# Performance work log

Hardware: AMD Instinct MI355X
Metric: run time of the kernel (lower is better)

The kernel has to match this reference:

```python
import jax, jax.numpy as jnp
import numpy as np
import math

HID = 768
HEADS = 12
HEAD_DIM = HID // HEADS
B, L = 64, 1024


def _xavier(key, shape):
    fan_in, fan_out = shape[0], shape[1]
    lim = math.sqrt(6.0 / (fan_in + fan_out))
    return jax.random.uniform(key, shape, jnp.float32, -lim, lim)


def setup_inputs() -> dict:
    key = jax.random.key(0)
    ks = jax.random.split(key, 12)
    inp = {
        "x_img": jax.random.normal(ks[0], (B, L, HID), jnp.float32),
        "cond": jax.random.normal(ks[1], (B, HID), jnp.float32),
        # attention projections
        "wq": _xavier(ks[2], (HID, HID)), "bq": jnp.zeros((HID,), jnp.float32),
        "wk": _xavier(ks[3], (HID, HID)), "bk": jnp.zeros((HID,), jnp.float32),
        "wv": _xavier(ks[4], (HID, HID)), "bv": jnp.zeros((HID,), jnp.float32),
        "wo": _xavier(ks[5], (HID, HID)), "bo": jnp.zeros((HID,), jnp.float32),
        # adaLN: zero-initialized in the original (keep small random so grads are non-trivial? No — stay faithful: zero init is the module's init, but zero would kill modulation. Use small random for a meaningful test.)
        "w_ada": jax.random.normal(ks[6], (HID, 6 * HID), jnp.float32) * 0.02,
        "b_ada": jnp.zeros((6 * HID,), jnp.float32),
        # MLP
        "w1": _xavier(ks[7], (HID, HID)), "b1": jnp.zeros((HID,), jnp.float32),
        "w2": _xavier(ks[8], (HID, HID)), "b2": jnp.zeros((HID,), jnp.float32),
        # LayerNorm params (norm_1: default scale=1, bias init const 1; norm_2: scale init const 1, bias default 0)
        "ln1_scale": jnp.ones((HID,), jnp.float32), "ln1_bias": jnp.ones((HID,), jnp.float32),
        "ln2_scale": jnp.ones((HID,), jnp.float32), "ln2_bias": jnp.zeros((HID,), jnp.float32),
    }
    return inp


def _layernorm(x, scale, bias, eps=1e-6):
    mu = jnp.mean(x, axis=-1, keepdims=True)
    var = jnp.var(x, axis=-1, keepdims=True)
    return (x - mu) * jax.lax.rsqrt(var + eps) * scale + bias


def _modulate(x, shift, scale):
    # shift/scale: [B, H] -> broadcast over seq axis
    return x * (1.0 + scale[:, None, :]) + shift[:, None, :]


def _attention(x, wq, bq, wk, bk, wv, bv, wo, bo):
    q = x @ wq + bq
    k = x @ wk + bk
    v = x @ wv + bv
    def split(t):
        b, l, _ = t.shape
        return t.reshape(b, l, HEADS, HEAD_DIM).transpose(0, 2, 1, 3)  # b h l d
    q, k, v = split(q), split(k), split(v)
    logits = jnp.einsum("bhqd,bhkd->bhqk", q, k) / math.sqrt(HEAD_DIM)
    attn = jax.nn.softmax(logits, axis=-1)
    out = jnp.einsum("bhqk,bhkd->bhqd", attn, v)
    out = out.transpose(0, 2, 1, 3).reshape(x.shape)  # b l (h d)
    return out @ wo + bo


def reference(x_img, cond, wq, bq, wk, bk, wv, bv, wo, bo, w_ada, b_ada,
              w1, b1, w2, b2, ln1_scale, ln1_bias, ln2_scale, ln2_bias):
    c = jax.nn.silu(cond) @ w_ada + b_ada  # [B, 6H]
    shift_msa, scale_msa, gate_msa, shift_mlp, scale_mlp, gate_mlp = jnp.split(c, 6, axis=1)

    h = _modulate(_layernorm(x_img, ln1_scale, ln1_bias), shift_msa, scale_msa)
    attn_out = _attention(h, wq, bq, wk, bk, wv, bv, wo, bo)
    x = x_img + gate_msa[:, None, :] * attn_out

    h2 = _modulate(_layernorm(x, ln2_scale, ln2_bias), shift_mlp, scale_mlp)
    mlp_out = jax.nn.silu(h2 @ w1 + b1) @ w2 + b2
    x = x + gate_mlp[:, None, :] * mlp_out
    return x
```

## Files before the change

### kernel.cpp

```cpp
#include <hip/hip_runtime.h>
#include <hip/hip_bf16.h>

typedef __bf16 bf16x8 __attribute__((ext_vector_type(8)));
typedef __bf16 bf16x4 __attribute__((ext_vector_type(4)));
typedef float  f32x4  __attribute__((ext_vector_type(4)));

#define MFMA_BF16(A_, B_, C_) __builtin_amdgcn_mfma_f32_16x16x32_bf16(A_, B_, C_, 0, 0, 0)

static constexpr int    HIDC  = 768;
static constexpr int    BB    = 64;
static constexpr int    LL    = 1024;
static constexpr int    MROWS = BB * LL;
static constexpr int    NHEAD = 12;
static constexpr int    HD    = 64;
static constexpr size_t QKV1  = (size_t)BB * NHEAD * LL * HD;
static constexpr float  QSCALE = 0.1803368801111204f;

static constexpr size_t OFF_WQKVT = 0;
static constexpr size_t OFF_WOT   = OFF_WQKVT + (size_t)2304 * 768 * 2;
static constexpr size_t OFF_W1T   = OFF_WOT   + (size_t)768 * 768 * 2;
static constexpr size_t OFF_W2T   = OFF_W1T   + (size_t)768 * 768 * 2;
static constexpr size_t OFF_BQKV  = OFF_W2T   + (size_t)768 * 768 * 2;
static constexpr size_t OFF_C     = OFF_BQKV  + (size_t)2304 * 4;
static constexpr size_t OFF_H     = OFF_C     + (size_t)64 * 4608 * 4;
static constexpr size_t OFF_AO    = OFF_H     + (size_t)MROWS * HIDC * 2;
static constexpr size_t OFF_QKV   = OFF_AO    + (size_t)MROWS * HIDC * 2;

__device__ __forceinline__ void async16(const __bf16* g, __bf16* l) {
    __builtin_amdgcn_global_load_lds((const __attribute__((address_space(1))) void*)g,
                                     (__attribute__((address_space(3))) void*)l, 16, 0, 0);
}

#define PH_BARRIER() do { __builtin_amdgcn_sched_barrier(0); asm volatile("" ::: "memory"); \
    __builtin_amdgcn_s_barrier(); asm volatile("" ::: "memory"); __builtin_amdgcn_sched_barrier(0); } while (0)
#define SYNC() do { asm volatile("" ::: "memory"); __builtin_amdgcn_s_barrier(); \
                    asm volatile("" ::: "memory"); } while (0)

__global__ __launch_bounds__(256) void tcvt6_k(const float* __restrict__ s0, const float* __restrict__ s1,
                                               const float* __restrict__ s2, const float* __restrict__ s3,
                                               const float* __restrict__ s4, const float* __restrict__ s5,
                                               __bf16* __restrict__ dbase) {
    __shared__ float t[64][65];
    const int bid = blockIdx.x;
    const int widx = bid / 144;
    const int tb = bid - widx * 144;
    const int kt = tb / 12, nt = tb - kt * 12;
    const float* src = (widx == 0) ? s0 : (widx == 1) ? s1 : (widx == 2) ? s2
                     : (widx == 3) ? s3 : (widx == 4) ? s4 : s5;
    const int tid = threadIdx.x;
    const int r = tid >> 4, c4 = (tid & 15) * 4;
    #pragma unroll
    for (int i = 0; i < 4; ++i) {
        const float4 v = *(const float4*)(src + (size_t)(kt * 64 + r + 16 * i) * 768 + nt * 64 + c4);
        t[r + 16 * i][c4 + 0] = v.x; t[r + 16 * i][c4 + 1] = v.y;
        t[r + 16 * i][c4 + 2] = v.z; t[r + 16 * i][c4 + 3] = v.w;
    }
    __syncthreads();
    const int n = tid >> 2, kg = (tid & 3) * 8;
    #pragma unroll
    for (int i = 0; i < 2; ++i) {
        const int k = kg + i * 32;
        bf16x8 o;
        #pragma unroll
        for (int j = 0; j < 8; ++j) o[j] = (__bf16)t[k + j][n];
        *(bf16x8*)(dbase + (size_t)widx * 768 * 768 + (size_t)(nt * 64 + n) * 768 + kt * 64 + k) = o;
    }
}

__global__ __launch_bounds__(256) void bcat_k(const float* __restrict__ bq, const float* __restrict__ bk,
                                              const float* __restrict__ bv, float* __restrict__ bqkv) {
    int i = blockIdx.x * 256 + threadIdx.x;
    if (i < 2304) {
        int w = i / 768, r = i - w * 768;
        const float* p = (w == 0) ? bq : (w == 1) ? bk : bv;
        bqkv[i] = p[r];
    }
}

__global__ __launch_bounds__(256) void ada_k(const float* __restrict__ cond, const float* __restrict__ w_ada,
                                             const float* __restrict__ b_ada, float* __restrict__ c) {
    __shared__ float s[8][768];
    const int tid = threadIdx.x;
    const int bt = blockIdx.x / 18;
    const int nt = blockIdx.x % 18;
    #pragma unroll
    for (int i = 0; i < 24; ++i) {
        int idx = i * 256 + tid;
        int bb = idx / 768, kk = idx - bb * 768;
        float v = cond[(size_t)(bt * 8 + bb) * 768 + kk];
        s[bb][kk] = v / (1.f + __expf(-v));
    }
    __syncthreads();
    const int n = nt * 256 + tid;
    float acc[8];
    #pragma unroll
    for (int j = 0; j < 8; ++j) acc[j] = 0.f;
    for (int k = 0; k < 768; ++k) {
        float w = w_ada[(size_t)k * 4608 + n];
        #pragma unroll
        for (int j = 0; j < 8; ++j) acc[j] += s[j][k] * w;
    }
    float bias = b_ada[n];
    #pragma unroll
    for (int j = 0; j < 8; ++j) c[(size_t)(bt * 8 + j) * 4608 + n] = acc[j] + bias;
}

__global__ __launch_bounds__(256) void ln_mod_f4_k(const float* __restrict__ x,
                                                   const float* __restrict__ lns, const float* __restrict__ lnb,
                                                   const float* __restrict__ c, int shift_off, int scale_off,
                                                   __bf16* __restrict__ out) {
    const int wave = threadIdx.x >> 6, lane = threadIdx.x & 63;
    const int row = blockIdx.x * 4 + wave;
    const size_t base = (size_t)row * HIDC;
    const int b = row >> 10;
    float4 v[3];
    #pragma unroll
    for (int i = 0; i < 3; ++i) v[i] = *(const float4*)(x + base + (i * 64 + lane) * 4);
    float s = 0.f, ss = 0.f;
    #pragma unroll
    for (int i = 0; i < 3; ++i) {
        s  += v[i].x + v[i].y + v[i].z + v[i].w;
        ss += v[i].x * v[i].x + v[i].y * v[i].y + v[i].z * v[i].z + v[i].w * v[i].w;
    }
    #pragma unroll
    for (int off = 1; off < 64; off <<= 1) { s += __shfl_xor(s, off); ss += __shfl_xor(ss, off); }
    const float mu   = s * (1.f / 768.f);
    const float var  = ss * (1.f / 768.f) - mu * mu;
    const float rstd = rsqrtf(var + 1e-6f);
    const float* cb = c + (size_t)b * 4608;
    #pragma unroll
    for (int i = 0; i < 3; ++i) {
        bf16x4 o;
        const float vv[4] = {v[i].x, v[i].y, v[i].z, v[i].w};
        #pragma unroll
        for (int j = 0; j < 4; ++j) {
            const int col = (i * 64 + lane) * 4 + j;
            float val = (vv[j] - mu) * rstd * lns[col] + lnb[col];
            val = val * (1.f + cb[scale_off + col]) + cb[shift_off + col];
            o[j] = (__bf16)val;
        }
        *(bf16x4*)(out + base + (i * 64 + lane) * 4) = o;
    }
}

__global__ __launch_bounds__(256) void ln_mod_b_k(const __bf16* __restrict__ x,
                                                  const float* __restrict__ lns, const float* __restrict__ lnb,
                                                  const float* __restrict__ c, int shift_off, int scale_off,
                                                  __bf16* __restrict__ out) {
    const int wave = threadIdx.x >> 6, lane = threadIdx.x & 63;
    const int row = blockIdx.x * 4 + wave;
    const size_t base = (size_t)row * HIDC;
    const int b = row >> 10;
    float v[12];
    #pragma unroll
    for (int i = 0; i < 3; ++i) {
        const bf16x4 xv = *(const bf16x4*)(x + base + (i * 64 + lane) * 4);
        #pragma unroll
        for (int j = 0; j < 4; ++j) v[i * 4 + j] = (float)xv[j];
    }
    float s = 0.f, ss = 0.f;
    #pragma unroll
    for (int i = 0; i < 12; ++i) { s += v[i]; ss += v[i] * v[i]; }
    #pragma unroll
    for (int off = 1; off < 64; off <<= 1) { s += __shfl_xor(s, off); ss += __shfl_xor(ss, off); }
    const float mu   = s * (1.f / 768.f);
    const float var  = ss * (1.f / 768.f) - mu * mu;
    const float rstd = rsqrtf(var + 1e-6f);
    const float* cb = c + (size_t)b * 4608;
    #pragma unroll
    for (int i = 0; i < 3; ++i) {
        bf16x4 o;
        #pragma unroll
        for (int j = 0; j < 4; ++j) {
            const int col = (i * 64 + lane) * 4 + j;
            float val = (v[i * 4 + j] - mu) * rstd * lns[col] + lnb[col];
            val = val * (1.f + cb[scale_off + col]) + cb[shift_off + col];
            o[j] = (__bf16)val;
        }
        *(bf16x4*)(out + base + (i * 64 + lane) * 4) = o;
    }
}

template<int EPI>
__global__ __launch_bounds__(512, 2) void gemm256_k(const __bf16* __restrict__ A, const __bf16* __restrict__ BT,
                                                    const float* __restrict__ bias, int NBLK,
                                                    const float* __restrict__ e_res, const __bf16* __restrict__ e_resb,
                                                    const float* __restrict__ e_gate, void* __restrict__ out0) {
    constexpr int K = 768;
    constexpr int NKT = K / 64;
    __shared__ __attribute__((aligned(16))) unsigned char LDSB[131072];
    const int tid = threadIdx.x;
    const int nwg = gridDim.x;
    const int cpx = nwg >> 3;
    const int bid = blockIdx.x;
    const int swz = (bid & 7) * cpx + (bid >> 3);
    const int mb = swz / NBLK, nb = swz - mb * NBLK;
    const size_t m0 = (size_t)mb * 256;
    const int n0 = nb * 256;
    const int wave = tid >> 6, lane = tid & 63;
    const int wm = wave >> 2, wn = wave & 3;
    const int lr = lane & 15, lg = lane >> 4;

    int prow[2], pcol[2], pphys[2];
    #pragma unroll
    for (int i = 0; i < 2; ++i) {
        int p = (i * 512 + tid) * 16;
        prow[i]  = p >> 7;
        pcol[i]  = ((p & 127) ^ ((prow[i] & 7) << 4)) >> 1;
        pphys[i] = p;
    }
    auto STAGE = [&](const __bf16* gbase, size_t rowstart, int kt, int regoff) {
        #pragma unroll
        for (int i = 0; i < 2; ++i) {
            const __bf16* g = gbase + (rowstart + (size_t)prow[i]) * K + kt * 64 + pcol[i];
            async16(g, (__bf16*)(LDSB + regoff + pphys[i]));
        }
    };
    auto AFRAG = [&](int db, int mf, int ks) -> bf16x8 {
        const int row = mf * 16 + lr;
        const int ph = row * 128 + ((ks * 64 + lg * 16) ^ ((row & 7) << 4));
        return *(const bf16x8*)(LDSB + db * 65536 + wm * 16384 + ph);
    };
    auto BFRAG = [&](int db, int nf, int ks) -> bf16x8 {
        const int row = (wn & 1) * 64 + nf * 16 + lr;
        const int ph = row * 128 + ((ks * 64 + lg * 16) ^ ((row & 7) << 4));
        return *(const bf16x8*)(LDSB + db * 65536 + 32768 + (wn >> 1) * 16384 + ph);
    };

    f32x4 acc[8][4];
    #pragma unroll
    for (int i = 0; i < 8; ++i)
        #pragma unroll
        for (int j = 0; j < 4; ++j) acc[i][j] = (f32x4){0.f, 0.f, 0.f, 0.f};
    bf16x8 Af[4][2], Af2[4][2], Bf[4][2];

    STAGE(BT, (size_t)n0,       0, 32768);
    STAGE(BT, (size_t)n0 + 128, 0, 49152);
    STAGE(A,  m0,               0, 0);
    STAGE(A,  m0 + 128,         0, 16384);
    STAGE(BT, (size_t)n0,       1, 65536 + 32768);
    STAGE(BT, (size_t)n0 + 128, 1, 65536 + 49152);
    asm volatile("s_waitcnt vmcnt(4)" ::: "memory");
    PH_BARRIER();

    #pragma unroll 2
    for (int g = 0; g < NKT; ++g) {
        const int db = g & 1, dbn = db ^ 1;
        #pragma unroll
        for (int mf = 0; mf < 4; ++mf) { Af[mf][0] = AFRAG(db, mf, 0); Af[mf][1] = AFRAG(db, mf, 1); }
        #pragma unroll
        for (int nf = 0; nf < 4; ++nf) { Bf[nf][0] = BFRAG(db, nf, 0); Bf[nf][1] = BFRAG(db, nf, 1); }
        if (g + 1 < NKT) {
            STAGE(A, m0,       g + 1, dbn * 65536);
            STAGE(A, m0 + 128, g + 1, dbn * 65536 + 16384);
        }
        __builtin_amdgcn_s_setprio(1);
        #pragma unroll
        for (int ks = 0; ks < 2; ++ks)
            #pragma unroll
            for (int mf = 0; mf < 4; ++mf)
                #pragma unroll
                for (int nf = 0; nf < 4; ++nf)
                    acc[mf][nf] = MFMA_BF16(Af[mf][ks], Bf[nf][ks], acc[mf][nf]);
        __builtin_amdgcn_s_setprio(0);
        PH_BARRIER();
        #pragma unroll
        for (int mf = 0; mf < 4; ++mf) { Af2[mf][0] = AFRAG(db, mf + 4, 0); Af2[mf][1] = AFRAG(db, mf + 4, 1); }
        if (g + 2 < NKT) {
            STAGE(BT, (size_t)n0,       g + 2, db * 65536 + 32768);
            STAGE(BT, (size_t)n0 + 128, g + 2, db * 65536 + 49152);
        }
        __builtin_amdgcn_s_setprio(1);
        #pragma unroll
        for (int ks = 0; ks < 2; ++ks)
            #pragma unroll
            for (int mf = 0; mf < 4; ++mf)
                #pragma unroll
                for (int nf = 0; nf < 4; ++nf)
                    acc[mf + 4][nf] = MFMA_BF16(Af2[mf][ks], Bf[nf][ks], acc[mf + 4][nf]);
        __builtin_amdgcn_s_setprio(0);
        if (g < NKT - 2)       asm volatile("s_waitcnt vmcnt(4)" ::: "memory");
        else if (g == NKT - 2) asm volatile("s_waitcnt vmcnt(0)" ::: "memory");
        if (g + 1 < NKT) PH_BARRIER();
    }

    #pragma unroll
    for (int mf = 0; mf < 8; ++mf) {
        #pragma unroll
        for (int nf = 0; nf < 4; ++nf) {
            const int col = wn * 64 + nf * 16 + lr;
            const int n = n0 + col;
            const int row0 = wm * 128 + mf * 16 + lg * 4;
            const size_t mbase = m0 + row0;
            float v4[4];
            #pragma unroll
            for (int r = 0; r < 4; ++r) v4[r] = acc[mf][nf][r] + bias[n];
            if constexpr (EPI == 0) {
                const int which = n / 768, rem = n - which * 768;
                const int hh = rem >> 6, dd = rem & 63;
                const size_t bI = mbase >> 10;
                const size_t lI0 = mbase & 1023;
                if (which == 0) {
                    #pragma unroll
                    for (int r = 0; r < 4; ++r)
                        ((__bf16*)out0)[(((size_t)bI * NHEAD + hh) * LL + lI0 + r) * HD + dd] = (__bf16)(v4[r] * QSCALE);
                } else if (which == 1) {
                    #pragma unroll
                    for (int r = 0; r < 4; ++r)
                        ((__bf16*)out0)[QKV1 + (((size_t)bI * NHEAD + hh) * LL + lI0 + r) * HD + dd] = (__bf16)v4[r];
                } else {
                    const int tile = (int)(lI0 >> 6), kv = (int)(lI0 & 63);
                    const int ks = kv >> 5, r5 = kv & 31;
                    const int lgj = (r5 >> 2) & 3;
                    const int jb = (r5 >> 4) << 2;
                    const int of = dd >> 4, lr2 = dd & 15;
                    bf16x4 pk;
                    #pragma unroll
                    for (int r = 0; r < 4; ++r) pk[r] = (__bf16)v4[r];
                    *(bf16x4*)((__bf16*)out0 + 2 * QKV1 + ((size_t)bI * NHEAD + hh) * (LL * HD)
                               + (size_t)tile * 4096 + ((ks * 4 + of) * 64 + lgj * 16 + lr2) * 8 + jb) = pk;
                }
            } else {
                #pragma unroll
                for (int r = 0; r < 4; ++r) {
                    const size_t m = mbase + r;
                    if constexpr (EPI == 2) {
                        float sv = v4[r] / (1.f + __expf(-v4[r]));
                        ((__bf16*)out0)[m * HIDC + n] = (__bf16)sv;
                    } else if constexpr (EPI == 3) {
                        size_t bI = m >> 10;
                        float gg = e_gate[bI * 4608 + n];
                        ((__bf16*)out0)[m * HIDC + n] = (__bf16)(e_res[m * HIDC + n] + gg * v4[r]);
                    } else {
                        size_t bI = m >> 10;
                        float gg = e_gate[bI * 4608 + n];
                        ((float*)out0)[m * HIDC + n] = (float)e_resb[m * HIDC + n] + gg * v4[r];
                    }
                }
            }
        }
    }
}

__global__ __launch_bounds__(512, 4) void attn_k(const __bf16* __restrict__ qb, const __bf16* __restrict__ kb,
                                                 const __bf16* __restrict__ v2g, __bf16* __restrict__ out) {
    __shared__ __attribute__((aligned(16))) unsigned char LDSA[32768];
    const int nwg = gridDim.x;
    const int cpx = nwg >> 3;
    const int bid = blockIdx.x;
    const int swz = (bid & 7) * cpx + (bid >> 3);
    const int bh = swz >> 2;
    const int qt = swz & 3;
    const int b = bh / NHEAD, h = bh - b * NHEAD;
    const int tid = threadIdx.x;
    const int wave = tid >> 6, lane = tid & 63;
    const int lr = lane & 15, lg = lane >> 4;
    const size_t base = (size_t)bh * LL * HD;

    const int q0 = qt * 256 + wave * 32;
    bf16x8 qf[2][2];
    #pragma unroll
    for (int qi = 0; qi < 2; ++qi) {
        const __bf16* qrow = qb + base + (size_t)(q0 + qi * 16 + lr) * HD;
        qf[qi][0] = *(const bf16x8*)(qrow + lg * 8);
        qf[qi][1] = *(const bf16x8*)(qrow + 32 + lg * 8);
    }

    const int pp = tid * 16;
    const int krow = pp >> 7;
    const int kcol = (pp & 127) ^ ((krow & 7) << 4);
    auto STAGE = [&](int t) {
        unsigned char* Lb = LDSA + (t & 1) * 16384;
        const __bf16* gk = kb + base + (size_t)(t * 64 + krow) * HD + (kcol >> 1);
        async16(gk, (__bf16*)(Lb + pp));
        const __bf16* gv = v2g + base + (size_t)t * 4096 + (pp >> 1);
        async16(gv, (__bf16*)(Lb + 8192 + pp));
    };

    bf16x8 vones;
    #pragma unroll
    for (int j = 0; j < 8; ++j) vones[j] = (__bf16)1.0f;

    f32x4 acc[2][4];
    f32x4 accl[2];
    #pragma unroll
    for (int qi = 0; qi < 2; ++qi) {
        accl[qi] = (f32x4){0.f, 0.f, 0.f, 0.f};
        #pragma unroll
        for (int i = 0; i < 4; ++i) acc[qi][i] = (f32x4){0.f, 0.f, 0.f, 0.f};
    }

    STAGE(0);

    for (int t = 0; t < LL / 64; ++t) {
        asm volatile("s_waitcnt vmcnt(0)" ::: "memory");
        SYNC();
        if (t + 1 < LL / 64) STAGE(t + 1);
        const unsigned char* KB = LDSA + (t & 1) * 16384;
        const unsigned char* VB = KB + 8192;

        f32x4 s[2][4];
        __builtin_amdgcn_s_setprio(1);
        #pragma unroll
        for (int sf = 0; sf < 4; ++sf) {
            const int row = sf * 16 + lr;
            const bf16x8 kf0 = *(const bf16x8*)(KB + row * 128 + ((lg * 16) ^ ((row & 7) << 4)));
            const bf16x8 kf1 = *(const bf16x8*)(KB + row * 128 + ((64 + lg * 16) ^ ((row & 7) << 4)));
            #pragma unroll
            for (int qi = 0; qi < 2; ++qi) {
                f32x4 tt = (f32x4){0.f, 0.f, 0.f, 0.f};
                tt = MFMA_BF16(kf0, qf[qi][0], tt);
                tt = MFMA_BF16(kf1, qf[qi][1], tt);
                s[qi][sf] = tt;
            }
        }
        __builtin_amdgcn_s_setprio(0);
        #pragma unroll
        for (int ks = 0; ks < 2; ++ks) {
            bf16x8 pb[2];
            #pragma unroll
            for (int qi = 0; qi < 2; ++qi) {
                #pragma unroll
                for (int j = 0; j < 4; ++j) {
                    pb[qi][j]     = (__bf16)exp2f(s[qi][2 * ks][j]);
                    pb[qi][4 + j] = (__bf16)exp2f(s[qi][2 * ks + 1][j]);
                }
                accl[qi] = MFMA_BF16(vones, pb[qi], accl[qi]);
            }
            __builtin_amdgcn_s_setprio(1);
            #pragma unroll
            for (int of = 0; of < 4; ++of) {
                const bf16x8 vf = *(const bf16x8*)(VB + ((ks * 4 + of) * 64 + lane) * 16);
                #pragma unroll
                for (int qi = 0; qi < 2; ++qi)
                    acc[qi][of] = MFMA_BF16(vf, pb[qi], acc[qi][of]);
            }
            __builtin_amdgcn_s_setprio(0);
        }
    }
    #pragma unroll
    for (int qi = 0; qi < 2; ++qi) {
        const float inv = 1.f / accl[qi][0];
        const int qq = q0 + qi * 16 + lr;
        #pragma unroll
        for (int of = 0; of < 4; ++of) {
            bf16x4 o;
            #pragma unroll
            for (int r = 0; r < 4; ++r) o[r] = (__bf16)(acc[qi][of][r] * inv);
            *(bf16x4*)(out + ((size_t)b * LL + qq) * HIDC + h * HD + of * 16 + lg * 4) = o;
        }
    }
}

extern "C" void kernel_launch(void* const* d_in, const int* in_sizes, int n_in,
                              void* d_out, int out_size, void* d_ws, size_t ws_size,
                              hipStream_t stream) {
    const float* x_img = (const float*)d_in[0];
    const float* cond  = (const float*)d_in[1];
    const float* wq    = (const float*)d_in[2];
    const float* bq    = (const float*)d_in[3];
    const float* wk    = (const float*)d_in[4];
    const float* bk    = (const float*)d_in[5];
    const float* wv    = (const float*)d_in[6];
    const float* bv    = (const float*)d_in[7];
    const float* wo    = (const float*)d_in[8];
    const float* bo    = (const float*)d_in[9];
    const float* w_ada = (const float*)d_in[10];
    const float* b_ada = (const float*)d_in[11];
    const float* w1    = (const float*)d_in[12];
    const float* b1    = (const float*)d_in[13];
    const float* w2    = (const float*)d_in[14];
    const float* b2    = (const float*)d_in[15];
    const float* ln1s  = (const float*)d_in[16];
    const float* ln1b  = (const float*)d_in[17];
    const float* ln2s  = (const float*)d_in[18];
    const float* ln2b  = (const float*)d_in[19];

    char* ws = (char*)d_ws;
    __bf16* wqkvT = (__bf16*)(ws + OFF_WQKVT);
    __bf16* woT   = (__bf16*)(ws + OFF_WOT);
    __bf16* w1T   = (__bf16*)(ws + OFF_W1T);
    __bf16* w2T   = (__bf16*)(ws + OFF_W2T);
    float*  bqkv  = (float*)(ws + OFF_BQKV);
    float*  cbuf  = (float*)(ws + OFF_C);
    __bf16* hbuf  = (__bf16*)(ws + OFF_H);
    __bf16* aobuf = (__bf16*)(ws + OFF_AO);
    __bf16* qkv   = (__bf16*)(ws + OFF_QKV);
    __bf16* xbuf  = (__bf16*)(ws + OFF_QKV);

    dim3 blk(256);
    dim3 blk512(512);

    tcvt6_k<<<6 * 144, blk, 0, stream>>>(wq, wk, wv, wo, w1, w2, wqkvT);
    bcat_k<<<9, blk, 0, stream>>>(bq, bk, bv, bqkv);
    ada_k<<<144, blk, 0, stream>>>(cond, w_ada, b_ada, cbuf);

    ln_mod_f4_k<<<MROWS / 4, blk, 0, stream>>>(x_img, ln1s, ln1b, cbuf, 0, 768, hbuf);

    gemm256_k<0><<<2304, blk512, 0, stream>>>(hbuf, wqkvT, bqkv, 9, nullptr, nullptr, nullptr, (void*)qkv);

    attn_k<<<BB * NHEAD * 4, blk512, 0, stream>>>(qkv, qkv + QKV1, qkv + 2 * QKV1, aobuf);

    gemm256_k<3><<<768, blk512, 0, stream>>>(aobuf, woT, bo, 3, x_img, nullptr, cbuf + 2 * 768, (void*)xbuf);

    ln_mod_b_k<<<MROWS / 4, blk, 0, stream>>>(xbuf, ln2s, ln2b, cbuf, 3 * 768, 4 * 768, hbuf);

    gemm256_k<2><<<768, blk512, 0, stream>>>(hbuf, w1T, b1, 3, nullptr, nullptr, nullptr, (void*)aobuf);

    gemm256_k<4><<<768, blk512, 0, stream>>>(aobuf, w2T, b2, 3, nullptr, xbuf, cbuf + 5 * 768, d_out);

    (void)in_sizes; (void)n_in; (void)out_size; (void)ws_size;
}
```

Baseline: 1.085 ms.

## Use 128x128 GEMM tiles for N=768 GEMMs and smaller attention blocks

Adds a 256-thread GEMM kernel with 128x128 tiles, a K-step of 32 and simple double buffering. The output, MLP1 and MLP2 projections now use it, giving 3072 workgroups instead of 768 so the CUs fill better and the tail is smaller. The 256-tile kernel is kept only for the QKV projection. Attention blocks shrink to 4 waves covering 128 queries each, with twice the grid and s_setprio hints removed. The cost is less operand reuse per tile, a shallower pipeline with full vmcnt(0) waits, and K/V tiles loaded twice as often across attention blocks.

```diff
diff --git a/kernel.cpp b/kernel.cpp
--- a/kernel.cpp
+++ b/kernel.cpp
@@ -33,8 +33,6 @@
 
 #define PH_BARRIER() do { __builtin_amdgcn_sched_barrier(0); asm volatile("" ::: "memory"); \
     __builtin_amdgcn_s_barrier(); asm volatile("" ::: "memory"); __builtin_amdgcn_sched_barrier(0); } while (0)
-#define SYNC() do { asm volatile("" ::: "memory"); __builtin_amdgcn_s_barrier(); \
-                    asm volatile("" ::: "memory"); } while (0)
 
 __global__ __launch_bounds__(256) void tcvt6_k(const float* __restrict__ s0, const float* __restrict__ s1,
                                                const float* __restrict__ s2, const float* __restrict__ s3,
@@ -184,8 +182,7 @@
 template<int EPI>
 __global__ __launch_bounds__(512, 2) void gemm256_k(const __bf16* __restrict__ A, const __bf16* __restrict__ BT,
                                                     const float* __restrict__ bias, int NBLK,
-                                                    const float* __restrict__ e_res, const __bf16* __restrict__ e_resb,
-                                                    const float* __restrict__ e_gate, void* __restrict__ out0) {
+                                                    void* __restrict__ out0) {
     constexpr int K = 768;
     constexpr int NKT = K / 64;
     __shared__ __attribute__((aligned(16))) unsigned char LDSB[131072];
@@ -295,69 +292,161 @@
             float v4[4];
             #pragma unroll
             for (int r = 0; r < 4; ++r) v4[r] = acc[mf][nf][r] + bias[n];
-            if constexpr (EPI == 0) {
-                const int which = n / 768, rem = n - which * 768;
-                const int hh = rem >> 6, dd = rem & 63;
-                const size_t bI = mbase >> 10;
-                const size_t lI0 = mbase & 1023;
-                if (which == 0) {
-                    #pragma unroll
-                    for (int r = 0; r < 4; ++r)
-                        ((__bf16*)out0)[(((size_t)bI * NHEAD + hh) * LL + lI0 + r) * HD + dd] = (__bf16)(v4[r] * QSCALE);
-                } else if (which == 1) {
-                    #pragma unroll
-                    for (int r = 0; r < 4; ++r)
-                        ((__bf16*)out0)[QKV1 + (((size_t)bI * NHEAD + hh) * LL + lI0 + r) * HD + dd] = (__bf16)v4[r];
+            const int which = n / 768, rem = n - which * 768;
+            const int hh = rem >> 6, dd = rem & 63;
+            const size_t bI = mbase >> 10;
+            const size_t lI0 = mbase & 1023;
+            if (which == 0) {
+                #pragma unroll
+                for (int r = 0; r < 4; ++r)
+                    ((__bf16*)out0)[(((size_t)bI * NHEAD + hh) * LL + lI0 + r) * HD + dd] = (__bf16)(v4[r] * QSCALE);
+            } else if (which == 1) {
+                #pragma unroll
+                for (int r = 0; r < 4; ++r)
+                    ((__bf16*)out0)[QKV1 + (((size_t)bI * NHEAD + hh) * LL + lI0 + r) * HD + dd] = (__bf16)v4[r];
+            } else {
+                const int tile = (int)(lI0 >> 6), kv = (int)(lI0 & 63);
+                const int ks = kv >> 5, r5 = kv & 31;
+                const int lgj = (r5 >> 2) & 3;
+                const int jb = (r5 >> 4) << 2;
+                const int of = dd >> 4, lr2 = dd & 15;
+                bf16x4 pk;
+                #pragma unroll
+                for (int r = 0; r < 4; ++r) pk[r] = (__bf16)v4[r];
+                *(bf16x4*)((__bf16*)out0 + 2 * QKV1 + ((size_t)bI * NHEAD + hh) * (LL * HD)
+                           + (size_t)tile * 4096 + ((ks * 4 + of) * 64 + lgj * 16 + lr2) * 8 + jb) = pk;
+            }
+        }
+    }
+}
+
+template<int EPI>
+__global__ __launch_bounds__(256, 2) void gemm128_k(const __bf16* __restrict__ A, const __bf16* __restrict__ BT,
+                                                    const float* __restrict__ bias, int NBLK,
+                                                    const float* __restrict__ e_res, const __bf16* __restrict__ e_resb,
+                                                    const float* __restrict__ e_gate, void* __restrict__ out0) {
+    constexpr int K = 768;
+    constexpr int NKT = K / 32;
+    __shared__ __attribute__((aligned(16))) unsigned char LDSB[32768];
+    const int tid = threadIdx.x;
+    const int nwg = gridDim.x;
+    const int cpx = nwg >> 3;
+    const int bid = blockIdx.x;
+    const int swz = (bid & 7) * cpx + (bid >> 3);
+    const int mb = swz / NBLK, nb = swz - mb * NBLK;
+    const size_t m0 = (size_t)mb * 128;
+    const int n0 = nb * 128;
+    const int wave = tid >> 6, lane = tid & 63;
+    const int wm = wave >> 1, wn = wave & 1;
+    const int lr = lane & 15, lg = lane >> 4;
+
+    int prow[2], pcol[2], pphys[2];
+    #pragma unroll
+    for (int i = 0; i < 2; ++i) {
+        int p = (i * 256 + tid) * 16;
+        prow[i]  = p >> 6;
+        pcol[i]  = ((p & 63) ^ (((prow[i] >> 1) & 3) << 4)) >> 1;
+        pphys[i] = p;
+    }
+    auto STAGE = [&](const __bf16* gbase, size_t rowstart, int kt, int dstoff) {
+        #pragma unroll
+        for (int i = 0; i < 2; ++i) {
+            const __bf16* g = gbase + (rowstart + (size_t)prow[i]) * K + kt * 32 + pcol[i];
+            async16(g, (__bf16*)(LDSB + dstoff + pphys[i]));
+        }
+    };
+    auto AFRAG = [&](int db, int mf) -> bf16x8 {
+        const int row = wm * 64 + mf * 16 + lr;
+        const int ph = row * 64 + ((lg * 16) ^ (((row >> 1) & 3) << 4));
+        return *(const bf16x8*)(LDSB + db * 16384 + ph);
+    };
+    auto BFRAG = [&](int db, int nf) -> bf16x8 {
+        const int row = wn * 64 + nf * 16 + lr;
+        const int ph = row * 64 + ((lg * 16) ^ (((row >> 1) & 3) << 4));
+        return *(const bf16x8*)(LDSB + db * 16384 + 8192 + ph);
+    };
+
+    f32x4 acc[4][4];
+    #pragma unroll
+    for (int i = 0; i < 4; ++i)
+        #pragma unroll
+        for (int j = 0; j < 4; ++j) acc[i][j] = (f32x4){0.f, 0.f, 0.f, 0.f};
+    bf16x8 Af[4], Bf[4];
+
+    STAGE(A,  m0,         0, 0);
+    STAGE(BT, (size_t)n0, 0, 8192);
+    asm volatile("s_waitcnt vmcnt(0)" ::: "memory");
+    PH_BARRIER();
+
+    #pragma unroll 2
+    for (int g = 0; g < NKT; ++g) {
+        const int db = g & 1, dbn = db ^ 1;
+        #pragma unroll
+        for (int mf = 0; mf < 4; ++mf) Af[mf] = AFRAG(db, mf);
+        #pragma unroll
+        for (int nf = 0; nf < 4; ++nf) Bf[nf] = BFRAG(db, nf);
+        if (g + 1 < NKT) {
+            STAGE(A,  m0,         g + 1, dbn * 16384);
+            STAGE(BT, (size_t)n0, g + 1, dbn * 16384 + 8192);
+        }
+        __builtin_amdgcn_s_setprio(1);
+        #pragma unroll
+        for (int mf = 0; mf < 4; ++mf)
+            #pragma unroll
+            for (int nf = 0; nf < 4; ++nf)
+                acc[mf][nf] = MFMA_BF16(Af[mf], Bf[nf], acc[mf][nf]);
+        __builtin_amdgcn_s_setprio(0);
+        asm volatile("s_waitcnt vmcnt(0)" ::: "memory");
+        if (g + 1 < NKT) PH_BARRIER();
+    }
+
+    #pragma unroll
+    for (int mf = 0; mf < 4; ++mf) {
+        #pragma unroll
+        for (int nf = 0; nf < 4; ++nf) {
+            const int col = wn * 64 + nf * 16 + lr;
+            const int n = n0 + col;
+            const int row0 = wm * 64 + mf * 16 + lg * 4;
+            const size_t mbase = m0 + row0;
+            float v4[4];
+            #pragma unroll
+            for (int r = 0; r < 4; ++r) v4[r] = acc[mf][nf][r] + bias[n];
+            #pragma unroll
+            for (int r = 0; r < 4; ++r) {
+                const size_t m = mbase + r;
+                if constexpr (EPI == 2) {
+                    float sv = v4[r] / (1.f + __expf(-v4[r]));
+                    ((__bf16*)out0)[m * HIDC + n] = (__bf16)sv;
+                } else if constexpr (EPI == 3) {
+                    size_t bI = m >> 10;
+                    float gg = e_gate[bI * 4608 + n];
+                    ((__bf16*)out0)[m * HIDC + n] = (__bf16)(e_res[m * HIDC + n] + gg * v4[r]);
                 } else {
-                    const int tile = (int)(lI0 >> 6), kv = (int)(lI0 & 63);
-                    const int ks = kv >> 5, r5 = kv & 31;
-                    const int lgj = (r5 >> 2) & 3;
-                    const int jb = (r5 >> 4) << 2;
-                    const int of = dd >> 4, lr2 = dd & 15;
-                    bf16x4 pk;
-                    #pragma unroll
-                    for (int r = 0; r < 4; ++r) pk[r] = (__bf16)v4[r];
-                    *(bf16x4*)((__bf16*)out0 + 2 * QKV1 + ((size_t)bI * NHEAD + hh) * (LL * HD)
-                               + (size_t)tile * 4096 + ((ks * 4 + of) * 64 + lgj * 16 + lr2) * 8 + jb) = pk;
-                }
-            } else {
-                #pragma unroll
-                for (int r = 0; r < 4; ++r) {
-                    const size_t m = mbase + r;
-                    if constexpr (EPI == 2) {
-                        float sv = v4[r] / (1.f + __expf(-v4[r]));
-                        ((__bf16*)out0)[m * HIDC + n] = (__bf16)sv;
-                    } else if constexpr (EPI == 3) {
-                        size_t bI = m >> 10;
-                        float gg = e_gate[bI * 4608 + n];
-                        ((__bf16*)out0)[m * HIDC + n] = (__bf16)(e_res[m * HIDC + n] + gg * v4[r]);
-                    } else {
-                        size_t bI = m >> 10;
-                        float gg = e_gate[bI * 4608 + n];
-                        ((float*)out0)[m * HIDC + n] = (float)e_resb[m * HIDC + n] + gg * v4[r];
-                    }
+                    size_t bI = m >> 10;
+                    float gg = e_gate[bI * 4608 + n];
+                    ((float*)out0)[m * HIDC + n] = (float)e_resb[m * HIDC + n] + gg * v4[r];
                 }
             }
         }
     }
 }
 
-__global__ __launch_bounds__(512, 4) void attn_k(const __bf16* __restrict__ qb, const __bf16* __restrict__ kb,
+__global__ __launch_bounds__(256, 4) void attn_k(const __bf16* __restrict__ qb, const __bf16* __restrict__ kb,
                                                  const __bf16* __restrict__ v2g, __bf16* __restrict__ out) {
     __shared__ __attribute__((aligned(16))) unsigned char LDSA[32768];
     const int nwg = gridDim.x;
     const int cpx = nwg >> 3;
     const int bid = blockIdx.x;
     const int swz = (bid & 7) * cpx + (bid >> 3);
-    const int bh = swz >> 2;
-    const int qt = swz & 3;
+    const int bh = swz >> 3;
+    const int qt = swz & 7;
     const int b = bh / NHEAD, h = bh - b * NHEAD;
     const int tid = threadIdx.x;
     const int wave = tid >> 6, lane = tid & 63;
     const int lr = lane & 15, lg = lane >> 4;
     const size_t base = (size_t)bh * LL * HD;
 
-    const int q0 = qt * 256 + wave * 32;
+    const int q0 = qt * 128 + wave * 32;
     bf16x8 qf[2][2];
     #pragma unroll
     for (int qi = 0; qi < 2; ++qi) {
@@ -365,16 +454,29 @@
         qf[qi][0] = *(const bf16x8*)(qrow + lg * 8);
         qf[qi][1] = *(const bf16x8*)(qrow + 32 + lg * 8);
     }
-
-    const int pp = tid * 16;
-    const int krow = pp >> 7;
-    const int kcol = (pp & 127) ^ ((krow & 7) << 4);
+    __builtin_amdgcn_sched_barrier(0);
+
+    int krow[2], kcol[2];
+    #pragma unroll
+    for (int i = 0; i < 2; ++i) {
+        int pp = (i * 256 + tid) * 16;
+        krow[i] = pp >> 7;
+        kcol[i] = (pp & 127) ^ ((krow[i] & 7) << 4);
+    }
     auto STAGE = [&](int t) {
         unsigned char* Lb = LDSA + (t & 1) * 16384;
-        const __bf16* gk = kb + base + (size_t)(t * 64 + krow) * HD + (kcol >> 1);
-        async16(gk, (__bf16*)(Lb + pp));
-        const __bf16* gv = v2g + base + (size_t)t * 4096 + (pp >> 1);
-        async16(gv, (__bf16*)(Lb + 8192 + pp));
+        const int kv0 = t * 64;
+        #pragma unroll
+        for (int i = 0; i < 2; ++i) {
+            const __bf16* g = kb + base + (size_t)(kv0 + krow[i]) * HD + (kcol[i] >> 1);
+            async16(g, (__bf16*)(Lb + (i * 256 + tid) * 16));
+        }
+        #pragma unroll
+        for (int i = 0; i < 2; ++i) {
+            int pp = (i * 256 + tid) * 16;
+            const __bf16* g = v2g + base + (size_t)t * 4096 + (pp >> 1);
+            async16(g, (__bf16*)(Lb + 8192 + pp));
+        }
     };
 
     bf16x8 vones;
@@ -394,13 +496,12 @@
 
     for (int t = 0; t < LL / 64; ++t) {
         asm volatile("s_waitcnt vmcnt(0)" ::: "memory");
-        SYNC();
+        PH_BARRIER();
         if (t + 1 < LL / 64) STAGE(t + 1);
         const unsigned char* KB = LDSA + (t & 1) * 16384;
         const unsigned char* VB = KB + 8192;
 
         f32x4 s[2][4];
-        __builtin_amdgcn_s_setprio(1);
         #pragma unroll
         for (int sf = 0; sf < 4; ++sf) {
             const int row = sf * 16 + lr;
@@ -414,7 +515,6 @@
                 s[qi][sf] = tt;
             }
         }
-        __builtin_amdgcn_s_setprio(0);
         #pragma unroll
         for (int ks = 0; ks < 2; ++ks) {
             bf16x8 pb[2];
@@ -427,7 +527,6 @@
                 }
                 accl[qi] = MFMA_BF16(vones, pb[qi], accl[qi]);
             }
-            __builtin_amdgcn_s_setprio(1);
             #pragma unroll
             for (int of = 0; of < 4; ++of) {
                 const bf16x8 vf = *(const bf16x8*)(VB + ((ks * 4 + of) * 64 + lane) * 16);
@@ -435,7 +534,6 @@
                 for (int qi = 0; qi < 2; ++qi)
                     acc[qi][of] = MFMA_BF16(vf, pb[qi], acc[qi][of]);
             }
-            __builtin_amdgcn_s_setprio(0);
         }
     }
     #pragma unroll
@@ -497,17 +595,17 @@
 
     ln_mod_f4_k<<<MROWS / 4, blk, 0, stream>>>(x_img, ln1s, ln1b, cbuf, 0, 768, hbuf);
 
-    gemm256_k<0><<<2304, blk512, 0, stream>>>(hbuf, wqkvT, bqkv, 9, nullptr, nullptr, nullptr, (void*)qkv);
-
-    attn_k<<<BB * NHEAD * 4, blk512, 0, stream>>>(qkv, qkv + QKV1, qkv + 2 * QKV1, aobuf);
-
-    gemm256_k<3><<<768, blk512, 0, stream>>>(aobuf, woT, bo, 3, x_img, nullptr, cbuf + 2 * 768, (void*)xbuf);
+    gemm256_k<0><<<2304, blk512, 0, stream>>>(hbuf, wqkvT, bqkv, 9, (void*)qkv);
+
+    attn_k<<<BB * NHEAD * 8, blk, 0, stream>>>(qkv, qkv + QKV1, qkv + 2 * QKV1, aobuf);
+
+    gemm128_k<3><<<3072, blk, 0, stream>>>(aobuf, woT, bo, 6, x_img, nullptr, cbuf + 2 * 768, (void*)xbuf);
 
     ln_mod_b_k<<<MROWS / 4, blk, 0, stream>>>(xbuf, ln2s, ln2b, cbuf, 3 * 768, 4 * 768, hbuf);
 
-    gemm256_k<2><<<768, blk512, 0, stream>>>(hbuf, w1T, b1, 3, nullptr, nullptr, nullptr, (void*)aobuf);
-
-    gemm256_k<4><<<768, blk512, 0, stream>>>(aobuf, w2T, b2, 3, nullptr, xbuf, cbuf + 5 * 768, d_out);
+    gemm128_k<2><<<3072, blk, 0, stream>>>(hbuf, w1T, b1, 6, nullptr, nullptr, nullptr, (void*)aobuf);
+
+    gemm128_k<4><<<3072, blk, 0, stream>>>(aobuf, w2T, b2, 6, nullptr, xbuf, cbuf + 5 * 768, d_out);
 
     (void)in_sizes; (void)n_in; (void)out_size; (void)ws_size;
 }
```

Result: slower. 1.128 ms (+4.0%).

## Shrink attention workgroups to 4 waves with 128-query tiles

Applied to the files above, without the earlier changes.

The attention kernel now runs 256-thread workgroups covering 128 queries each instead of 512 threads covering 256, which doubles the grid. Each thread issues two async K and two async V loads per stage so the 16 KB tile is still filled. The wave priority hints are removed and the plain barrier becomes a scheduling-fenced barrier. Smaller groups should make barriers cheaper and give finer scheduling, but each K/V tile is now loaded by twice as many workgroups, doubling K/V global and LDS traffic.

```diff
diff --git a/kernel.cpp b/kernel.cpp
--- a/kernel.cpp
+++ b/kernel.cpp
@@ -33,8 +33,6 @@
 
 #define PH_BARRIER() do { __builtin_amdgcn_sched_barrier(0); asm volatile("" ::: "memory"); \
     __builtin_amdgcn_s_barrier(); asm volatile("" ::: "memory"); __builtin_amdgcn_sched_barrier(0); } while (0)
-#define SYNC() do { asm volatile("" ::: "memory"); __builtin_amdgcn_s_barrier(); \
-                    asm volatile("" ::: "memory"); } while (0)
 
 __global__ __launch_bounds__(256) void tcvt6_k(const float* __restrict__ s0, const float* __restrict__ s1,
                                                const float* __restrict__ s2, const float* __restrict__ s3,
@@ -342,22 +340,22 @@
     }
 }
 
-__global__ __launch_bounds__(512, 4) void attn_k(const __bf16* __restrict__ qb, const __bf16* __restrict__ kb,
+__global__ __launch_bounds__(256, 4) void attn_k(const __bf16* __restrict__ qb, const __bf16* __restrict__ kb,
                                                  const __bf16* __restrict__ v2g, __bf16* __restrict__ out) {
     __shared__ __attribute__((aligned(16))) unsigned char LDSA[32768];
     const int nwg = gridDim.x;
     const int cpx = nwg >> 3;
     const int bid = blockIdx.x;
     const int swz = (bid & 7) * cpx + (bid >> 3);
-    const int bh = swz >> 2;
-    const int qt = swz & 3;
+    const int bh = swz >> 3;
+    const int qt = swz & 7;
     const int b = bh / NHEAD, h = bh - b * NHEAD;
     const int tid = threadIdx.x;
     const int wave = tid >> 6, lane = tid & 63;
     const int lr = lane & 15, lg = lane >> 4;
     const size_t base = (size_t)bh * LL * HD;
 
-    const int q0 = qt * 256 + wave * 32;
+    const int q0 = qt * 128 + wave * 32;
     bf16x8 qf[2][2];
     #pragma unroll
     for (int qi = 0; qi < 2; ++qi) {
@@ -365,16 +363,29 @@
         qf[qi][0] = *(const bf16x8*)(qrow + lg * 8);
         qf[qi][1] = *(const bf16x8*)(qrow + 32 + lg * 8);
     }
-
-    const int pp = tid * 16;
-    const int krow = pp >> 7;
-    const int kcol = (pp & 127) ^ ((krow & 7) << 4);
+    __builtin_amdgcn_sched_barrier(0);
+
+    int krow[2], kcol[2];
+    #pragma unroll
+    for (int i = 0; i < 2; ++i) {
+        int pp = (i * 256 + tid) * 16;
+        krow[i] = pp >> 7;
+        kcol[i] = (pp & 127) ^ ((krow[i] & 7) << 4);
+    }
     auto STAGE = [&](int t) {
         unsigned char* Lb = LDSA + (t & 1) * 16384;
-        const __bf16* gk = kb + base + (size_t)(t * 64 + krow) * HD + (kcol >> 1);
-        async16(gk, (__bf16*)(Lb + pp));
-        const __bf16* gv = v2g + base + (size_t)t * 4096 + (pp >> 1);
-        async16(gv, (__bf16*)(Lb + 8192 + pp));
+        const int kv0 = t * 64;
+        #pragma unroll
+        for (int i = 0; i < 2; ++i) {
+            const __bf16* g = kb + base + (size_t)(kv0 + krow[i]) * HD + (kcol[i] >> 1);
+            async16(g, (__bf16*)(Lb + (i * 256 + tid) * 16));
+        }
+        #pragma unroll
+        for (int i = 0; i < 2; ++i) {
+            int pp = (i * 256 + tid) * 16;
+            const __bf16* g = v2g + base + (size_t)t * 4096 + (pp >> 1);
+            async16(g, (__bf16*)(Lb + 8192 + pp));
+        }
     };
 
     bf16x8 vones;
@@ -394,13 +405,12 @@
 
     for (int t = 0; t < LL / 64; ++t) {
         asm volatile("s_waitcnt vmcnt(0)" ::: "memory");
-        SYNC();
+        PH_BARRIER();
         if (t + 1 < LL / 64) STAGE(t + 1);
         const unsigned char* KB = LDSA + (t & 1) * 16384;
         const unsigned char* VB = KB + 8192;
 
         f32x4 s[2][4];
-        __builtin_amdgcn_s_setprio(1);
         #pragma unroll
         for (int sf = 0; sf < 4; ++sf) {
             const int row = sf * 16 + lr;
@@ -414,7 +424,6 @@
                 s[qi][sf] = tt;
             }
         }
-        __builtin_amdgcn_s_setprio(0);
         #pragma unroll
         for (int ks = 0; ks < 2; ++ks) {
             bf16x8 pb[2];
@@ -427,7 +436,6 @@
                 }
                 accl[qi] = MFMA_BF16(vones, pb[qi], accl[qi]);
             }
-            __builtin_amdgcn_s_setprio(1);
             #pragma unroll
             for (int of = 0; of < 4; ++of) {
                 const bf16x8 vf = *(const bf16x8*)(VB + ((ks * 4 + of) * 64 + lane) * 16);
@@ -435,7 +443,6 @@
                 for (int qi = 0; qi < 2; ++qi)
                     acc[qi][of] = MFMA_BF16(vf, pb[qi], acc[qi][of]);
             }
-            __builtin_amdgcn_s_setprio(0);
         }
     }
     #pragma unroll
@@ -499,7 +506,7 @@
 
     gemm256_k<0><<<2304, blk512, 0, stream>>>(hbuf, wqkvT, bqkv, 9, nullptr, nullptr, nullptr, (void*)qkv);
 
-    attn_k<<<BB * NHEAD * 4, blk512, 0, stream>>>(qkv, qkv + QKV1, qkv + 2 * QKV1, aobuf);
+    attn_k<<<BB * NHEAD * 8, blk, 0, stream>>>(qkv, qkv + QKV1, qkv + 2 * QKV1, aobuf);
 
     gemm256_k<3><<<768, blk512, 0, stream>>>(aobuf, woT, bo, 3, x_img, nullptr, cbuf + 2 * 768, (void*)xbuf);
 
```

New measurement: 1.082 ms. About the same (-0.3%).
